# Performance work log

Hardware: AMD Instinct MI355X
Metric: run time of the kernel (lower is better)

Reference implementation:

```python
import jax, jax.numpy as jnp
import numpy as np

# Transformer-XL relative multi-head attention (eval mode, dropout = identity)
B, Q, M, D, H = 2, 1024, 1024, 1024, 16
DH = D // H          # 64 head dim
K = Q + M            # key length = memory + current segment
SCALE = 0.02         # param init scale


def setup_inputs() -> dict:
    key = jax.random.key(0)
    ks = jax.random.split(key, 10)
    return {
        "inputs": jax.random.normal(ks[0], (B, Q, D), jnp.float32),
        "inputs_mem": jax.random.normal(ks[1], (B, M, D), jnp.float32),
        "r": jax.random.normal(ks[2], (B, K, D), jnp.float32),
        "W_qkv": jax.random.normal(ks[3], (D, 3 * D), jnp.float32) * SCALE,
        "b_qkv": jnp.zeros((3 * D,), jnp.float32),
        "W_r": jax.random.normal(ks[4], (D, D), jnp.float32) * SCALE,
        "b_r": jnp.zeros((D,), jnp.float32),
        "W_o": jax.random.normal(ks[5], (D, D), jnp.float32) * SCALE,
        "b_o": jnp.zeros((D,), jnp.float32),
        "u": jax.random.normal(ks[6], (1, H, 1, DH), jnp.float32) * SCALE,
        "v": jax.random.normal(ks[7], (1, H, 1, DH), jnp.float32) * SCALE,
    }


def _split_heads(x):
    # [B, L, D] -> [B, H, L, DH]
    b, l, _ = x.shape
    return x.reshape(b, l, H, DH).transpose(0, 2, 1, 3)


def _rel_shift(x):
    # Transformer-XL relative shift: pad one zero column on the left,
    # reshape to [B, H, K+1, Q], drop first row, reshape back.
    b, h, q, k = x.shape
    x = jnp.pad(x, ((0, 0), (0, 0), (0, 0), (1, 0)))
    x = x.reshape(b, h, k + 1, q)[:, :, 1:, :]
    return x.reshape(b, h, q, k)


def reference(inputs, inputs_mem, r, W_qkv, b_qkv, W_r, b_r, W_o, b_o, u, v):
    cat = jnp.concatenate([inputs_mem, inputs], axis=1)      # [B, K, D]
    w = cat @ W_qkv + b_qkv                                   # [B, K, 3D]
    rp = r @ W_r + b_r                                        # [B, K, D]
    # NOTE: source splits as (q, v, k) in that order
    w_q, w_v, w_k = jnp.split(w, 3, axis=-1)
    hq = _split_heads(w_q)[:, :, -Q:]                          # [B, H, Q, DH]
    hk = _split_heads(w_k)                                     # [B, H, K, DH]
    hv = _split_heads(w_v)                                     # [B, H, K, DH]
    hr = _split_heads(rp)                                      # [B, H, K, DH]
    ac = jnp.einsum('bhqd,bhkd->bhqk', hq + u, hk)             # content term
    bd = _rel_shift(jnp.einsum('bhqd,bhkd->bhqk', hq + v, hr)) # position term
    score = (ac + bd) / (DH ** 0.5)
    # causal mask with memory: query i attends to all mem + positions <= i
    mem_len = K - Q
    mask = (jnp.arange(K)[None, :] <= mem_len + jnp.arange(Q)[:, None]).astype(jnp.float32)
    score = score * mask - 1e30 * (1.0 - mask)
    weights = jax.nn.softmax(score, axis=-1)                   # [B, H, Q, K]
    out = jnp.einsum('bhqk,bhkd->bhqd', weights, hv)           # [B, H, Q, DH]
    out = out.transpose(0, 2, 1, 3).reshape(B, Q, D)
    return out @ W_o + b_o
```

## Files before the change

kernel.cpp:

```cpp
#include <hip/hip_runtime.h>
#include <hip/hip_bf16.h>
#include <stdint.h>


typedef __bf16 bf16;
typedef __bf16 bf16x2 __attribute__((ext_vector_type(2)));
typedef __bf16 bf16x4 __attribute__((ext_vector_type(4)));
typedef __bf16 bf16x8 __attribute__((ext_vector_type(8)));
typedef float  f32x4  __attribute__((ext_vector_type(4)));

__device__ __forceinline__ void async_copy16(void* lds, const void* g) {
    auto gp = (const __attribute__((address_space(1))) void*)(uintptr_t)g;
    auto lp = (__attribute__((address_space(3))) void*)(uint32_t)(uintptr_t)lds;
    __builtin_amdgcn_global_load_lds(gp, lp, 16, 0, 0);
}

__device__ __forceinline__ void gemm128_core(
    const bf16* __restrict__ A, const bf16* __restrict__ Bt, const int Kd,
    const int m0, const int n0, bf16* As, bf16* Bs, f32x4 acc[4][4])
{
    const int tid  = threadIdx.x;
    const int lane = tid & 63;
    const int wave = tid >> 6;
    const int wr   = (wave >> 1) * 64;
    const int wc   = (wave & 1) * 64;
    const int lr   = lane & 15;
    const int q4   = lane >> 4;

#pragma unroll
    for (int i = 0; i < 4; ++i)
#pragma unroll
        for (int j = 0; j < 4; ++j) {
            acc[i][j][0] = 0.f; acc[i][j][1] = 0.f; acc[i][j][2] = 0.f; acc[i][j][3] = 0.f;
        }

    for (int k0 = 0; k0 < Kd; k0 += 32) {
#pragma unroll
        for (int it = 0; it < 2; ++it) {
            const int cb0   = (it * 4 + wave) * 64;
            const int chunk = cb0 + lane;
            const int row   = chunk >> 2;
            const int cg    = (chunk & 3) * 8;
            async_copy16(As + cb0 * 8, A  + (size_t)(m0 + row) * Kd + k0 + cg);
            async_copy16(Bs + cb0 * 8, Bt + (size_t)(n0 + row) * Kd + k0 + cg);
        }
        __syncthreads();
        bf16x8 af[4], bfr[4];
#pragma unroll
        for (int rb = 0; rb < 4; ++rb)
            af[rb] = *(const bf16x8*)&As[(wr + rb * 16 + lr) * 32 + q4 * 8];
#pragma unroll
        for (int cb = 0; cb < 4; ++cb)
            bfr[cb] = *(const bf16x8*)&Bs[(wc + cb * 16 + lr) * 32 + q4 * 8];
#pragma unroll
        for (int rb = 0; rb < 4; ++rb)
#pragma unroll
            for (int cb = 0; cb < 4; ++cb)
                acc[rb][cb] = __builtin_amdgcn_mfma_f32_16x16x32_bf16(af[rb], bfr[cb], acc[rb][cb], 0, 0, 0);
        __syncthreads();
    }
}

__global__ __launch_bounds__(256) void k_tcast(const float* __restrict__ in,
                                               bf16* __restrict__ out, int R, int C)
{
    __shared__ float t[32][33];
    const int c0 = blockIdx.x * 32, r0 = blockIdx.y * 32;
    const int lc = threadIdx.x & 31, lrow = threadIdx.x >> 5;
#pragma unroll
    for (int p = 0; p < 4; ++p)
        t[lrow + p * 8][lc] = in[(size_t)(r0 + lrow + p * 8) * C + c0 + lc];
    __syncthreads();
#pragma unroll
    for (int p = 0; p < 4; ++p)
        out[(size_t)(c0 + lrow + p * 8) * R + r0 + lc] = (bf16)t[lc][lrow + p * 8];
}

__global__ __launch_bounds__(256) void k_cast_cat(const float* __restrict__ mem,
                                                  const float* __restrict__ inp,
                                                  bf16* __restrict__ catb)
{
    const int e   = (blockIdx.x * 256 + threadIdx.x) * 4;
    const int row = e >> 10, dc = e & 1023;
    const int b   = row >> 11, k = row & 2047;
    const float* src = (k < 1024) ? mem + ((size_t)b * 1024 + k) * 1024 + dc
                                  : inp + ((size_t)b * 1024 + (k - 1024)) * 1024 + dc;
    float4 f = *(const float4*)src;
    bf16x4 o; o[0] = (bf16)f.x; o[1] = (bf16)f.y; o[2] = (bf16)f.z; o[3] = (bf16)f.w;
    *(bf16x4*)&catb[e] = o;
}

__global__ __launch_bounds__(256) void k_cast(const float* __restrict__ in,
                                              bf16* __restrict__ out)
{
    const int e = (blockIdx.x * 256 + threadIdx.x) * 4;
    float4 f = *(const float4*)(in + e);
    bf16x4 o; o[0] = (bf16)f.x; o[1] = (bf16)f.y; o[2] = (bf16)f.z; o[3] = (bf16)f.w;
    *(bf16x4*)&out[e] = o;
}

__global__ __launch_bounds__(256) void k_gemm_qkv(
    const bf16* __restrict__ catb, const bf16* __restrict__ Wt,
    const float* __restrict__ bias, const float* __restrict__ u, const float* __restrict__ v,
    bf16* __restrict__ hq_u, bf16* __restrict__ hq_v,
    bf16* __restrict__ hk, bf16* __restrict__ hvT)
{
    __shared__ bf16 lds[2 * 128 * 32];
    f32x4 acc[4][4];
    const int m0 = blockIdx.x * 128, n0 = blockIdx.y * 128;
    gemm128_core(catb, Wt, 1024, m0, n0, lds, lds + 128 * 32, acc);

    const int lane = threadIdx.x & 63, wave = threadIdx.x >> 6;
    const int wr = (wave >> 1) * 64, wc = (wave & 1) * 64;
    const int lr = lane & 15, q4 = lane >> 4;
#pragma unroll
    for (int rb = 0; rb < 4; ++rb) {
#pragma unroll
        for (int cb = 0; cb < 4; ++cb) {
            const int col  = n0 + wc + cb * 16 + lr;
            const int part = col >> 10;
            const int hd   = col & 1023;
            const int h    = hd >> 6, d = hd & 63;
            const float bcol = bias[col];
#pragma unroll
            for (int r = 0; r < 4; ++r) {
                const int row = m0 + wr + rb * 16 + q4 * 4 + r;
                const int b   = row >> 11, k = row & 2047;
                const float val = acc[rb][cb][r] + bcol;
                if (part == 0) {
                    if (k >= 1024) {
                        const size_t o = (((size_t)(b * 16 + h)) * 1024 + (k - 1024)) * 64 + d;
                        hq_u[o] = (bf16)(val + u[hd]);
                        hq_v[o] = (bf16)(val + v[hd]);
                    }
                } else if (part == 1) {
                    hvT[(((size_t)(b * 16 + h)) * 64 + d) * 2048 + k] = (bf16)val;
                } else {
                    hk[(((size_t)(b * 16 + h)) * 2048 + k) * 64 + d] = (bf16)val;
                }
            }
        }
    }
}

__global__ __launch_bounds__(256) void k_gemm_r(
    const bf16* __restrict__ rb_, const bf16* __restrict__ Wt,
    const float* __restrict__ bias, bf16* __restrict__ hr)
{
    __shared__ bf16 lds[2 * 128 * 32];
    f32x4 acc[4][4];
    const int m0 = blockIdx.x * 128, n0 = blockIdx.y * 128;
    gemm128_core(rb_, Wt, 1024, m0, n0, lds, lds + 128 * 32, acc);

    const int lane = threadIdx.x & 63, wave = threadIdx.x >> 6;
    const int wr = (wave >> 1) * 64, wc = (wave & 1) * 64;
    const int lr = lane & 15, q4 = lane >> 4;
#pragma unroll
    for (int rb = 0; rb < 4; ++rb) {
#pragma unroll
        for (int cb = 0; cb < 4; ++cb) {
            const int col = n0 + wc + cb * 16 + lr;
            const int h = col >> 6, d = col & 63;
            const float bcol = bias[col];
#pragma unroll
            for (int r = 0; r < 4; ++r) {
                const int row = m0 + wr + rb * 16 + q4 * 4 + r;
                const int b = row >> 11, k = row & 2047;
                hr[(((size_t)(b * 16 + h)) * 2048 + k) * 64 + d] = (bf16)(acc[rb][cb][r] + bcol);
            }
        }
    }
}

__global__ __launch_bounds__(256) void k_gemm_out(
    const bf16* __restrict__ attn, const bf16* __restrict__ Wt,
    const float* __restrict__ bias, float* __restrict__ out)
{
    __shared__ bf16 lds[2 * 128 * 32];
    f32x4 acc[4][4];
    const int m0 = blockIdx.x * 128, n0 = blockIdx.y * 128;
    gemm128_core(attn, Wt, 1024, m0, n0, lds, lds + 128 * 32, acc);

    const int lane = threadIdx.x & 63, wave = threadIdx.x >> 6;
    const int wr = (wave >> 1) * 64, wc = (wave & 1) * 64;
    const int lr = lane & 15, q4 = lane >> 4;
#pragma unroll
    for (int rb = 0; rb < 4; ++rb) {
#pragma unroll
        for (int cb = 0; cb < 4; ++cb) {
            const int col = n0 + wc + cb * 16 + lr;
            const float bcol = bias[col];
#pragma unroll
            for (int r = 0; r < 4; ++r) {
                const int row = m0 + wr + rb * 16 + q4 * 4 + r;
                out[(size_t)row * 1024 + col] = acc[rb][cb][r] + bcol;
            }
        }
    }
}

__global__ __launch_bounds__(256) void k_attn(
    const bf16* __restrict__ hq_u, const bf16* __restrict__ hq_v,
    const bf16* __restrict__ hk, const bf16* __restrict__ hvT,
    const bf16* __restrict__ hr, bf16* __restrict__ attn)
{
    __shared__ bf16 Ks[64][72];
    __shared__ bf16 Vt[64][72];
    __shared__ bf16 Rs[128][72];
    __shared__ bf16 U[4][1344];

    const int bh = blockIdx.y;
    const int qt = (bh & 16) ? (15 - (int)blockIdx.x) : (int)blockIdx.x;
    const int q0 = qt * 64;
    const int tid = threadIdx.x, lane = tid & 63, wave = tid >> 6;
    const int lr = lane & 15, q4 = lane >> 4;
    bf16* Uw = &U[wave][0];

    const int nt = 17 + qt;
    const size_t kvbase = (size_t)bh * 2048 * 64;

    const int ci0  = tid,        r0_ = ci0 >> 3,  c0_ = (ci0 & 7) * 8;
    const int ci1  = 256 + tid,  r1_ = ci1 >> 3,  c1_ = (ci1 & 7) * 8;

    bf16x8 kv0, kv1, vv0, vv1, rv[4];
    auto load_tile = [&](int t) {
        const int k0 = t * 64;
        kv0 = *(const bf16x8*)&hk [kvbase + (size_t)(k0 + r0_) * 64 + c0_];
        kv1 = *(const bf16x8*)&hk [kvbase + (size_t)(k0 + r1_) * 64 + c1_];
        vv0 = *(const bf16x8*)&hvT[kvbase + (size_t)r0_ * 2048 + k0 + c0_];
        vv1 = *(const bf16x8*)&hvT[kvbase + (size_t)r1_ * 2048 + k0 + c1_];
        const int j0 = k0 + 1024 - q0 - 64;
#pragma unroll
        for (int p = 0; p < 4; ++p) {
            const int ci = p * 256 + tid;
            const int jrow = ci >> 3, cg = (ci & 7) * 8;
            const int j = j0 + jrow;
            bf16x8 val;
#pragma unroll
            for (int z = 0; z < 8; ++z) val[z] = (bf16)0.f;
            if (j < 2048) val = *(const bf16x8*)&hr[kvbase + (size_t)j * 64 + cg];
            rv[p] = val;
        }
    };
    auto write_tile = [&]() {
        *(bf16x8*)&Ks[r0_][c0_] = kv0;
        *(bf16x8*)&Ks[r1_][c1_] = kv1;
        *(bf16x8*)&Vt[r0_][c0_] = vv0;
        *(bf16x8*)&Vt[r1_][c1_] = vv1;
#pragma unroll
        for (int p = 0; p < 4; ++p) {
            const int ci = p * 256 + tid;
            *(bf16x8*)&Rs[ci >> 3][(ci & 7) * 8] = rv[p];
        }
    };

    const size_t qrow = ((size_t)bh * 1024 + q0 + wave * 16 + lr) * 64;
    const bf16x8 qu0 = *(const bf16x8*)&hq_u[qrow + q4 * 8];
    const bf16x8 qu1 = *(const bf16x8*)&hq_u[qrow + 32 + q4 * 8];
    const bf16x8 qv0 = *(const bf16x8*)&hq_v[qrow + q4 * 8];
    const bf16x8 qv1 = *(const bf16x8*)&hq_v[qrow + 32 + q4 * 8];

    f32x4 Oacc[4];
#pragma unroll
    for (int i = 0; i < 4; ++i) { Oacc[i][0] = 0.f; Oacc[i][1] = 0.f; Oacc[i][2] = 0.f; Oacc[i][3] = 0.f; }
    float lp[4] = {0.f, 0.f, 0.f, 0.f};

    load_tile(0);
    write_tile();
    __syncthreads();

    for (int t = 0; t < nt; ++t) {
        const int k0 = t * 64;
        const bool more = (t + 1 < nt);
        if (more) load_tile(t + 1);

        __builtin_amdgcn_s_setprio(1);
        f32x4 S[4];
#pragma unroll
        for (int cb = 0; cb < 4; ++cb) {
            const bf16x8 kf0 = *(const bf16x8*)&Ks[cb * 16 + lr][q4 * 8];
            const bf16x8 kf1 = *(const bf16x8*)&Ks[cb * 16 + lr][32 + q4 * 8];
            f32x4 z; z[0] = 0.f; z[1] = 0.f; z[2] = 0.f; z[3] = 0.f;
            z = __builtin_amdgcn_mfma_f32_16x16x32_bf16(qu0, kf0, z, 0, 0, 0);
            S[cb] = __builtin_amdgcn_mfma_f32_16x16x32_bf16(qu1, kf1, z, 0, 0, 0);
        }
#pragma unroll
        for (int jbi = 0; jbi < 5; ++jbi) {
            const int jb = jbi + 3 - wave;
            const bf16x8 rf0 = *(const bf16x8*)&Rs[jb * 16 + lr][q4 * 8];
            const bf16x8 rf1 = *(const bf16x8*)&Rs[jb * 16 + lr][32 + q4 * 8];
            f32x4 z; z[0] = 0.f; z[1] = 0.f; z[2] = 0.f; z[3] = 0.f;
            z = __builtin_amdgcn_mfma_f32_16x16x32_bf16(qv0, rf0, z, 0, 0, 0);
            z = __builtin_amdgcn_mfma_f32_16x16x32_bf16(qv1, rf1, z, 0, 0, 0);
#pragma unroll
            for (int r = 0; r < 4; ++r) Uw[(q4 * 4 + r) * 84 + jbi * 16 + lr] = (bf16)z[r];
        }

        float bdv[4][4];
#pragma unroll
        for (int cb = 0; cb < 4; ++cb)
#pragma unroll
            for (int r = 0; r < 4; ++r) {
                const int tq = q4 * 4 + r;
                bdv[cb][r] = (float)Uw[tq * 84 + cb * 16 + lr + 15 - tq];
            }

#pragma unroll
        for (int cb = 0; cb < 4; ++cb) {
            const int k = k0 + cb * 16 + lr;
#pragma unroll
            for (int r = 0; r < 4; ++r) {
                const int q = q0 + wave * 16 + q4 * 4 + r;
                const float s = (S[cb][r] + bdv[cb][r]) * 0.125f;
                const float p = (k <= 1024 + q) ? __expf(s) : 0.f;
                lp[r] += p;
                Uw[(q4 * 4 + r) * 76 + cb * 16 + lr] = (bf16)p;
            }
        }

        const bf16x8 pf0 = *(const bf16x8*)&Uw[lr * 76 + q4 * 8];
        const bf16x8 pf1 = *(const bf16x8*)&Uw[lr * 76 + 32 + q4 * 8];
#pragma unroll
        for (int db = 0; db < 4; ++db) {
            const bf16x8 vf0 = *(const bf16x8*)&Vt[db * 16 + lr][q4 * 8];
            const bf16x8 vf1 = *(const bf16x8*)&Vt[db * 16 + lr][32 + q4 * 8];
            Oacc[db] = __builtin_amdgcn_mfma_f32_16x16x32_bf16(pf0, vf0, Oacc[db], 0, 0, 0);
            Oacc[db] = __builtin_amdgcn_mfma_f32_16x16x32_bf16(pf1, vf1, Oacc[db], 0, 0, 0);
        }
        __builtin_amdgcn_s_setprio(0);

        if (more) {
            __syncthreads();
            write_tile();
            __syncthreads();
        }
    }

#pragma unroll
    for (int off = 1; off < 16; off <<= 1)
#pragma unroll
        for (int r = 0; r < 4; ++r) lp[r] += __shfl_xor(lp[r], off, 64);

    const int b = bh >> 4, h = bh & 15;
#pragma unroll
    for (int r = 0; r < 4; ++r) {
        const float rl = 1.f / lp[r];
        const int q = q0 + wave * 16 + q4 * 4 + r;
#pragma unroll
        for (int db = 0; db < 4; ++db) {
            const int d = db * 16 + lr;
            attn[(((size_t)b * 1024 + q) * 16 + h) * 64 + d] = (bf16)(Oacc[db][r] * rl);
        }
    }
}

extern "C" void kernel_launch(void* const* d_in, const int* in_sizes, int n_in,
                              void* d_out, int out_size, void* d_ws, size_t ws_size,
                              hipStream_t stream)
{
    const float* inputs = (const float*)d_in[0];
    const float* mem    = (const float*)d_in[1];
    const float* r      = (const float*)d_in[2];
    const float* W_qkv  = (const float*)d_in[3];
    const float* b_qkv  = (const float*)d_in[4];
    const float* W_r    = (const float*)d_in[5];
    const float* b_r    = (const float*)d_in[6];
    const float* W_o    = (const float*)d_in[7];
    const float* b_o    = (const float*)d_in[8];
    const float* u      = (const float*)d_in[9];
    const float* v      = (const float*)d_in[10];
    float* out = (float*)d_out;

    char* ws = (char*)d_ws;
    size_t off = 0;
    auto alloc = [&](size_t bytes) -> void* {
        void* p = ws + off;
        off += (bytes + 255) & ~(size_t)255;
        return p;
    };
    bf16* hq_u  = (bf16*)alloc(2ull * 16 * 1024 * 64 * 2);
    bf16* hq_v  = (bf16*)alloc(2ull * 16 * 1024 * 64 * 2);
    bf16* hk    = (bf16*)alloc(2ull * 16 * 2048 * 64 * 2);
    bf16* hvT   = (bf16*)alloc(2ull * 16 * 2048 * 64 * 2);
    bf16* hr    = (bf16*)alloc(2ull * 16 * 2048 * 64 * 2);
    bf16* attnb = (bf16*)alloc(2ull * 1024 * 1024 * 2);
    bf16* Wot   = (bf16*)alloc(1024ull * 1024 * 2);
    bf16* catb  = (bf16*)alloc(4096ull * 1024 * 2);
    bf16* rb    = (bf16*)alloc(4096ull * 1024 * 2);
    bf16* Wqkvt = (bf16*)alloc(3072ull * 1024 * 2);
    bf16* Wrt   = (bf16*)alloc(1024ull * 1024 * 2);

    k_tcast<<<dim3(96, 32), 256, 0, stream>>>(W_qkv, Wqkvt, 1024, 3072);
    k_tcast<<<dim3(32, 32), 256, 0, stream>>>(W_r, Wrt, 1024, 1024);
    k_tcast<<<dim3(32, 32), 256, 0, stream>>>(W_o, Wot, 1024, 1024);
    k_cast_cat<<<4096, 256, 0, stream>>>(mem, inputs, catb);
    k_cast<<<4096, 256, 0, stream>>>(r, rb);

    k_gemm_qkv<<<dim3(32, 24), 256, 0, stream>>>(catb, Wqkvt, b_qkv, u, v, hq_u, hq_v, hk, hvT);
    k_gemm_r<<<dim3(32, 8), 256, 0, stream>>>(rb, Wrt, b_r, hr);
    k_attn<<<dim3(16, 32), 256, 0, stream>>>(hq_u, hq_v, hk, hvT, hr, attnb);
    k_gemm_out<<<dim3(16, 8), 256, 0, stream>>>(attnb, Wot, b_o, out);
}
```

Measured before the change: 287.0 us.

## Merge QKV and R projections; double-buffer attention K/V and ring-buffer R tiles

The QKV and positional projection GEMMs are merged into one launch, using a grid branch on blockIdx.y, so the R projection fills the same wave of blocks instead of running as a separate small kernel. In the attention kernel, K/V tiles are now double-buffered and the relative-position R tile is held in a three-slot ring of 64-row chunks. Each iteration then loads only one new R chunk instead of reloading 128 rows, and one of the two barriers per iteration is dropped. The cost is more LDS per block, which may reduce occupancy, plus extra index arithmetic for the ring slots.

```diff
diff --git a/kernel.cpp b/kernel.cpp
--- a/kernel.cpp
+++ b/kernel.cpp
@@ -99,74 +99,68 @@
     *(bf16x4*)&out[e] = o;
 }
 
-__global__ __launch_bounds__(256) void k_gemm_qkv(
-    const bf16* __restrict__ catb, const bf16* __restrict__ Wt,
-    const float* __restrict__ bias, const float* __restrict__ u, const float* __restrict__ v,
+__global__ __launch_bounds__(256) void k_gemm_qkvr(
+    const bf16* __restrict__ catb, const bf16* __restrict__ Wqkvt,
+    const float* __restrict__ b_qkv, const float* __restrict__ u, const float* __restrict__ v,
+    const bf16* __restrict__ rb_, const bf16* __restrict__ Wrt,
+    const float* __restrict__ b_r,
     bf16* __restrict__ hq_u, bf16* __restrict__ hq_v,
-    bf16* __restrict__ hk, bf16* __restrict__ hvT)
+    bf16* __restrict__ hk, bf16* __restrict__ hvT, bf16* __restrict__ hr)
 {
     __shared__ bf16 lds[2 * 128 * 32];
     f32x4 acc[4][4];
-    const int m0 = blockIdx.x * 128, n0 = blockIdx.y * 128;
-    gemm128_core(catb, Wt, 1024, m0, n0, lds, lds + 128 * 32, acc);
-
+    const int m0 = blockIdx.x * 128;
     const int lane = threadIdx.x & 63, wave = threadIdx.x >> 6;
     const int wr = (wave >> 1) * 64, wc = (wave & 1) * 64;
     const int lr = lane & 15, q4 = lane >> 4;
-#pragma unroll
-    for (int rb = 0; rb < 4; ++rb) {
-#pragma unroll
-        for (int cb = 0; cb < 4; ++cb) {
-            const int col  = n0 + wc + cb * 16 + lr;
-            const int part = col >> 10;
-            const int hd   = col & 1023;
-            const int h    = hd >> 6, d = hd & 63;
-            const float bcol = bias[col];
-#pragma unroll
-            for (int r = 0; r < 4; ++r) {
-                const int row = m0 + wr + rb * 16 + q4 * 4 + r;
-                const int b   = row >> 11, k = row & 2047;
-                const float val = acc[rb][cb][r] + bcol;
-                if (part == 0) {
-                    if (k >= 1024) {
-                        const size_t o = (((size_t)(b * 16 + h)) * 1024 + (k - 1024)) * 64 + d;
-                        hq_u[o] = (bf16)(val + u[hd]);
-                        hq_v[o] = (bf16)(val + v[hd]);
+
+    if (blockIdx.y < 24) {
+        const int n0 = blockIdx.y * 128;
+        gemm128_core(catb, Wqkvt, 1024, m0, n0, lds, lds + 128 * 32, acc);
+#pragma unroll
+        for (int rb = 0; rb < 4; ++rb) {
+#pragma unroll
+            for (int cb = 0; cb < 4; ++cb) {
+                const int col  = n0 + wc + cb * 16 + lr;
+                const int part = col >> 10;
+                const int hd   = col & 1023;
+                const int h    = hd >> 6, d = hd & 63;
+                const float bcol = b_qkv[col];
+#pragma unroll
+                for (int r = 0; r < 4; ++r) {
+                    const int row = m0 + wr + rb * 16 + q4 * 4 + r;
+                    const int b   = row >> 11, k = row & 2047;
+                    const float val = acc[rb][cb][r] + bcol;
+                    if (part == 0) {
+                        if (k >= 1024) {
+                            const size_t o = (((size_t)(b * 16 + h)) * 1024 + (k - 1024)) * 64 + d;
+                            hq_u[o] = (bf16)(val + u[hd]);
+                            hq_v[o] = (bf16)(val + v[hd]);
+                        }
+                    } else if (part == 1) {
+                        hvT[(((size_t)(b * 16 + h)) * 64 + d) * 2048 + k] = (bf16)val;
+                    } else {
+                        hk[(((size_t)(b * 16 + h)) * 2048 + k) * 64 + d] = (bf16)val;
                     }
-                } else if (part == 1) {
-                    hvT[(((size_t)(b * 16 + h)) * 64 + d) * 2048 + k] = (bf16)val;
-                } else {
-                    hk[(((size_t)(b * 16 + h)) * 2048 + k) * 64 + d] = (bf16)val;
                 }
             }
         }
-    }
-}
-
-__global__ __launch_bounds__(256) void k_gemm_r(
-    const bf16* __restrict__ rb_, const bf16* __restrict__ Wt,
-    const float* __restrict__ bias, bf16* __restrict__ hr)
-{
-    __shared__ bf16 lds[2 * 128 * 32];
-    f32x4 acc[4][4];
-    const int m0 = blockIdx.x * 128, n0 = blockIdx.y * 128;
-    gemm128_core(rb_, Wt, 1024, m0, n0, lds, lds + 128 * 32, acc);
-
-    const int lane = threadIdx.x & 63, wave = threadIdx.x >> 6;
-    const int wr = (wave >> 1) * 64, wc = (wave & 1) * 64;
-    const int lr = lane & 15, q4 = lane >> 4;
-#pragma unroll
-    for (int rb = 0; rb < 4; ++rb) {
-#pragma unroll
-        for (int cb = 0; cb < 4; ++cb) {
-            const int col = n0 + wc + cb * 16 + lr;
-            const int h = col >> 6, d = col & 63;
-            const float bcol = bias[col];
-#pragma unroll
-            for (int r = 0; r < 4; ++r) {
-                const int row = m0 + wr + rb * 16 + q4 * 4 + r;
-                const int b = row >> 11, k = row & 2047;
-                hr[(((size_t)(b * 16 + h)) * 2048 + k) * 64 + d] = (bf16)(acc[rb][cb][r] + bcol);
+    } else {
+        const int n0 = (blockIdx.y - 24) * 128;
+        gemm128_core(rb_, Wrt, 1024, m0, n0, lds, lds + 128 * 32, acc);
+#pragma unroll
+        for (int rb = 0; rb < 4; ++rb) {
+#pragma unroll
+            for (int cb = 0; cb < 4; ++cb) {
+                const int col = n0 + wc + cb * 16 + lr;
+                const int h = col >> 6, d = col & 63;
+                const float bcol = b_r[col];
+#pragma unroll
+                for (int r = 0; r < 4; ++r) {
+                    const int row = m0 + wr + rb * 16 + q4 * 4 + r;
+                    const int b = row >> 11, k = row & 2047;
+                    hr[(((size_t)(b * 16 + h)) * 2048 + k) * 64 + d] = (bf16)(acc[rb][cb][r] + bcol);
+                }
             }
         }
     }
@@ -204,9 +198,9 @@
     const bf16* __restrict__ hk, const bf16* __restrict__ hvT,
     const bf16* __restrict__ hr, bf16* __restrict__ attn)
 {
-    __shared__ bf16 Ks[64][72];
-    __shared__ bf16 Vt[64][72];
-    __shared__ bf16 Rs[128][72];
+    __shared__ bf16 Ks[2][64][72];
+    __shared__ bf16 Vt[2][64][72];
+    __shared__ bf16 Rs[192 * 72];
     __shared__ bf16 U[4][1344];
 
     const int bh = blockIdx.y;
@@ -216,42 +210,39 @@
     const int lr = lane & 15, q4 = lane >> 4;
     bf16* Uw = &U[wave][0];
 
-    const int nt = 17 + qt;
+    const int nt  = 17 + qt;
+    const int m0c = 15 - qt;
     const size_t kvbase = (size_t)bh * 2048 * 64;
 
     const int ci0  = tid,        r0_ = ci0 >> 3,  c0_ = (ci0 & 7) * 8;
     const int ci1  = 256 + tid,  r1_ = ci1 >> 3,  c1_ = (ci1 & 7) * 8;
 
-    bf16x8 kv0, kv1, vv0, vv1, rv[4];
-    auto load_tile = [&](int t) {
+    bf16x8 kv0, kv1, vv0, vv1, rv0, rv1;
+    auto load_kv = [&](int t) {
         const int k0 = t * 64;
         kv0 = *(const bf16x8*)&hk [kvbase + (size_t)(k0 + r0_) * 64 + c0_];
         kv1 = *(const bf16x8*)&hk [kvbase + (size_t)(k0 + r1_) * 64 + c1_];
         vv0 = *(const bf16x8*)&hvT[kvbase + (size_t)r0_ * 2048 + k0 + c0_];
         vv1 = *(const bf16x8*)&hvT[kvbase + (size_t)r1_ * 2048 + k0 + c1_];
-        const int j0 = k0 + 1024 - q0 - 64;
-#pragma unroll
-        for (int p = 0; p < 4; ++p) {
-            const int ci = p * 256 + tid;
-            const int jrow = ci >> 3, cg = (ci & 7) * 8;
-            const int j = j0 + jrow;
-            bf16x8 val;
-#pragma unroll
-            for (int z = 0; z < 8; ++z) val[z] = (bf16)0.f;
-            if (j < 2048) val = *(const bf16x8*)&hr[kvbase + (size_t)j * 64 + cg];
-            rv[p] = val;
-        }
     };
-    auto write_tile = [&]() {
-        *(bf16x8*)&Ks[r0_][c0_] = kv0;
-        *(bf16x8*)&Ks[r1_][c1_] = kv1;
-        *(bf16x8*)&Vt[r0_][c0_] = vv0;
-        *(bf16x8*)&Vt[r1_][c1_] = vv1;
-#pragma unroll
-        for (int p = 0; p < 4; ++p) {
-            const int ci = p * 256 + tid;
-            *(bf16x8*)&Rs[ci >> 3][(ci & 7) * 8] = rv[p];
-        }
+    auto load_r = [&](int c) {
+        if (c * 64 < 2048) {
+            rv0 = *(const bf16x8*)&hr[kvbase + (size_t)(c * 64 + r0_) * 64 + c0_];
+            rv1 = *(const bf16x8*)&hr[kvbase + (size_t)(c * 64 + r1_) * 64 + c1_];
+        } else {
+#pragma unroll
+            for (int z = 0; z < 8; ++z) { rv0[z] = (bf16)0.f; rv1[z] = (bf16)0.f; }
+        }
+    };
+    auto write_kv = [&](int buf) {
+        *(bf16x8*)&Ks[buf][r0_][c0_] = kv0;
+        *(bf16x8*)&Ks[buf][r1_][c1_] = kv1;
+        *(bf16x8*)&Vt[buf][r0_][c0_] = vv0;
+        *(bf16x8*)&Vt[buf][r1_][c1_] = vv1;
+    };
+    auto write_r = [&](int slot) {
+        *(bf16x8*)&Rs[(slot * 64 + r0_) * 72 + c0_] = rv0;
+        *(bf16x8*)&Rs[(slot * 64 + r1_) * 72 + c1_] = rv1;
     };
 
     const size_t qrow = ((size_t)bh * 1024 + q0 + wave * 16 + lr) * 64;
@@ -265,30 +256,37 @@
     for (int i = 0; i < 4; ++i) { Oacc[i][0] = 0.f; Oacc[i][1] = 0.f; Oacc[i][2] = 0.f; Oacc[i][3] = 0.f; }
     float lp[4] = {0.f, 0.f, 0.f, 0.f};
 
-    load_tile(0);
-    write_tile();
+    load_kv(0);  write_kv(0);
+    load_r(m0c);     write_r(m0c % 3);
+    load_r(m0c + 1); write_r((m0c + 1) % 3);
     __syncthreads();
 
     for (int t = 0; t < nt; ++t) {
-        const int k0 = t * 64;
+        const int k0  = t * 64;
+        const int mt  = m0c + t;
+        const int s0  = mt % 3;
+        const int s1  = (s0 + 1 == 3) ? 0 : s0 + 1;
+        const int s2  = (s1 + 1 == 3) ? 0 : s1 + 1;
+        const int buf = t & 1;
         const bool more = (t + 1 < nt);
-        if (more) load_tile(t + 1);
+        if (more) { load_kv(t + 1); load_r(mt + 2); }
 
         __builtin_amdgcn_s_setprio(1);
         f32x4 S[4];
 #pragma unroll
         for (int cb = 0; cb < 4; ++cb) {
-            const bf16x8 kf0 = *(const bf16x8*)&Ks[cb * 16 + lr][q4 * 8];
-            const bf16x8 kf1 = *(const bf16x8*)&Ks[cb * 16 + lr][32 + q4 * 8];
+            const bf16x8 kf0 = *(const bf16x8*)&Ks[buf][cb * 16 + lr][q4 * 8];
+            const bf16x8 kf1 = *(const bf16x8*)&Ks[buf][cb * 16 + lr][32 + q4 * 8];
             f32x4 z; z[0] = 0.f; z[1] = 0.f; z[2] = 0.f; z[3] = 0.f;
             z = __builtin_amdgcn_mfma_f32_16x16x32_bf16(qu0, kf0, z, 0, 0, 0);
             S[cb] = __builtin_amdgcn_mfma_f32_16x16x32_bf16(qu1, kf1, z, 0, 0, 0);
         }
 #pragma unroll
         for (int jbi = 0; jbi < 5; ++jbi) {
-            const int jb = jbi + 3 - wave;
-            const bf16x8 rf0 = *(const bf16x8*)&Rs[jb * 16 + lr][q4 * 8];
-            const bf16x8 rf1 = *(const bf16x8*)&Rs[jb * 16 + lr][32 + q4 * 8];
+            const int jb   = jbi + 3 - wave;
+            const int rrow = ((jb & 4) ? s1 : s0) * 64 + (jb & 3) * 16 + lr;
+            const bf16x8 rf0 = *(const bf16x8*)&Rs[rrow * 72 + q4 * 8];
+            const bf16x8 rf1 = *(const bf16x8*)&Rs[rrow * 72 + 32 + q4 * 8];
             f32x4 z; z[0] = 0.f; z[1] = 0.f; z[2] = 0.f; z[3] = 0.f;
             z = __builtin_amdgcn_mfma_f32_16x16x32_bf16(qv0, rf0, z, 0, 0, 0);
             z = __builtin_amdgcn_mfma_f32_16x16x32_bf16(qv1, rf1, z, 0, 0, 0);
@@ -322,16 +320,16 @@
         const bf16x8 pf1 = *(const bf16x8*)&Uw[lr * 76 + 32 + q4 * 8];
 #pragma unroll
         for (int db = 0; db < 4; ++db) {
-            const bf16x8 vf0 = *(const bf16x8*)&Vt[db * 16 + lr][q4 * 8];
-            const bf16x8 vf1 = *(const bf16x8*)&Vt[db * 16 + lr][32 + q4 * 8];
+            const bf16x8 vf0 = *(const bf16x8*)&Vt[buf][db * 16 + lr][q4 * 8];
+            const bf16x8 vf1 = *(const bf16x8*)&Vt[buf][db * 16 + lr][32 + q4 * 8];
             Oacc[db] = __builtin_amdgcn_mfma_f32_16x16x32_bf16(pf0, vf0, Oacc[db], 0, 0, 0);
             Oacc[db] = __builtin_amdgcn_mfma_f32_16x16x32_bf16(pf1, vf1, Oacc[db], 0, 0, 0);
         }
         __builtin_amdgcn_s_setprio(0);
 
         if (more) {
-            __syncthreads();
-            write_tile();
+            write_kv(buf ^ 1);
+            write_r(s2);
             __syncthreads();
         }
     }
@@ -396,8 +394,9 @@
     k_cast_cat<<<4096, 256, 0, stream>>>(mem, inputs, catb);
     k_cast<<<4096, 256, 0, stream>>>(r, rb);
 
-    k_gemm_qkv<<<dim3(32, 24), 256, 0, stream>>>(catb, Wqkvt, b_qkv, u, v, hq_u, hq_v, hk, hvT);
-    k_gemm_r<<<dim3(32, 8), 256, 0, stream>>>(rb, Wrt, b_r, hr);
+    k_gemm_qkvr<<<dim3(32, 32), 256, 0, stream>>>(catb, Wqkvt, b_qkv, u, v,
+                                                  rb, Wrt, b_r,
+                                                  hq_u, hq_v, hk, hvT, hr);
     k_attn<<<dim3(16, 32), 256, 0, stream>>>(hq_u, hq_v, hk, hvT, hr, attnb);
     k_gemm_out<<<dim3(16, 8), 256, 0, stream>>>(attnb, Wot, b_o, out);
 }
```

New measurement: 272.3 us. 1.05x faster.
